# Performance work log

Measured on AMD Instinct MI355X. Metric: run time of the kernel, lower is better.

## Reference

```python
import math
import jax, jax.numpy as jnp
import numpy as np

NUM_HEAD = 16
BLOCK_SIZE = 2048

def get_slopes(n):
    def pow2(n):
        start = 2 ** (-2 ** (-(math.log2(n) - 3)))
        return [start * start ** i for i in range(n)]
    if math.log2(n).is_integer():
        return pow2(n)
    c = 2 ** math.floor(math.log2(n))
    return pow2(c) + get_slopes(2 * c)[0::2][: n - c]

def setup_inputs() -> dict:
    key = jax.random.key(0)
    ks = jax.random.split(key, 5)
    B, T, C = 4, 2048, 1024
    x = jax.random.normal(ks[0], (B, T, C), dtype=jnp.float32)
    Wq = 0.02 * jax.random.normal(ks[1], (C, C), dtype=jnp.float32)
    Wk = 0.02 * jax.random.normal(ks[2], (C, C), dtype=jnp.float32)
    Wv = 0.02 * jax.random.normal(ks[3], (C, C), dtype=jnp.float32)
    Wo = 0.02 * jax.random.normal(ks[4], (C, C), dtype=jnp.float32)
    return {"x": x, "Wq": Wq, "Wk": Wk, "Wv": Wv, "Wo": Wo}

def reference(x, Wq, Wk, Wv, Wo):
    B, T, C = x.shape
    nh, hd = NUM_HEAD, C // NUM_HEAD
    # projections, split heads -> [B, nh, T, hd]
    q = (x @ Wq).reshape(B, T, nh, hd).transpose(0, 2, 1, 3)
    k = (x @ Wk).reshape(B, T, nh, hd).transpose(0, 2, 1, 3)
    v = (x @ Wv).reshape(B, T, nh, hd).transpose(0, 2, 1, 3)
    # full [B, nh, T, T] scores (module materializes these)
    attn = jnp.einsum("bhqd,bhkd->bhqk", q, k) / jnp.sqrt(jnp.float32(hd))
    # ALiBi bias as in create_mask: slope * (j - (block_size - 1)), key-position only
    slopes = jnp.asarray(get_slopes(nh), dtype=jnp.float32)  # [nh]
    bias = slopes[:, None] * (jnp.arange(T, dtype=jnp.float32) - (BLOCK_SIZE - 1))  # [nh, T]
    attn = attn + bias[None, :, None, :]
    # causal mask + stable softmax in fp32
    causal = jnp.tril(jnp.ones((T, T), dtype=bool))
    masked = jnp.where(causal[None, None], attn.astype(jnp.float32), jnp.finfo(jnp.float32).min)
    probs = jax.nn.softmax(masked, axis=-1)
    out = jnp.einsum("bhqk,bhkd->bhqd", probs, v)  # [B, nh, T, hd]
    out = out.transpose(0, 2, 1, 3).reshape(B, T, C)
    return out @ Wo
```

## Files before the change

kernel.cpp:

```cpp
#include <hip/hip_runtime.h>
#include <hip/hip_bf16.h>

#define TSEQ   2048
#define CDIM   1024
#define NHEAD  16
#define HDIM   64

typedef float f32x4  __attribute__((ext_vector_type(4)));
typedef float f32x16v __attribute__((ext_vector_type(16)));
typedef __bf16 bf16x8 __attribute__((ext_vector_type(8)));
typedef unsigned short u16x8 __attribute__((ext_vector_type(8)));
typedef unsigned short u16x4 __attribute__((ext_vector_type(4)));
typedef unsigned int   u32x4 __attribute__((ext_vector_type(4)));

#define QSCALE 0.18033688011112042f
#define LOG2E  1.4426950408889634f

static __device__ __forceinline__ unsigned short f2bf(float f) {
    unsigned u = __builtin_bit_cast(unsigned, f);
    unsigned r = u + 0x7FFFu + ((u >> 16) & 1u);
    return (unsigned short)(r >> 16);
}

static __device__ __forceinline__ f32x4 mfma16(u16x8 a, u16x8 b, f32x4 c) {
    return __builtin_amdgcn_mfma_f32_16x16x32_bf16(
        __builtin_bit_cast(bf16x8, a), __builtin_bit_cast(bf16x8, b), c, 0, 0, 0);
}
static __device__ __forceinline__ f32x16v mfma32(u16x8 a, u16x8 b, f32x16v c) {
    return __builtin_amdgcn_mfma_f32_32x32x16_bf16(
        __builtin_bit_cast(bf16x8, a), __builtin_bit_cast(bf16x8, b), c, 0, 0, 0);
}

static __device__ __forceinline__ void gload16(const void* g, void* l) {
    __builtin_amdgcn_global_load_lds(
        (const __attribute__((address_space(1))) unsigned int*)g,
        (__attribute__((address_space(3))) unsigned int*)l, 16, 0, 0);
}


__global__ __launch_bounds__(256) void castx(
    const float* __restrict__ x, unsigned short* __restrict__ xb)
{
    int t = blockIdx.x * 256 + threadIdx.x;
    f32x4 v = *(const f32x4*)&x[t * 4];
    u16x4 o;
    o[0] = f2bf(v[0]); o[1] = f2bf(v[1]); o[2] = f2bf(v[2]); o[3] = f2bf(v[3]);
    *(u16x4*)&xb[t * 4] = o;
}

__global__ __launch_bounds__(256) void wtcast(
    const float* __restrict__ wq, const float* __restrict__ wk,
    const float* __restrict__ wv, const float* __restrict__ wo,
    unsigned short* __restrict__ wt)
{
    __shared__ unsigned short t[64 * 72];
    const int z = blockIdx.z;
    const float* src = (z == 0) ? wq : (z == 1) ? wk : (z == 2) ? wv : wo;
    const int k0 = blockIdx.x * 64, n0 = blockIdx.y * 64, tid = threadIdx.x;

    #pragma unroll
    for (int i = 0; i < 4; ++i) {
        int idx = i * 256 + tid;
        int r = idx >> 4, c4 = idx & 15;
        f32x4 v = *(const f32x4*)&src[(k0 + r) * 1024 + n0 + c4 * 4];
        u16x4 o;
        o[0] = f2bf(v[0]); o[1] = f2bf(v[1]); o[2] = f2bf(v[2]); o[3] = f2bf(v[3]);
        *(u16x4*)&t[r * 72 + c4 * 4] = o;
    }
    __syncthreads();
    #pragma unroll
    for (int i = 0; i < 2; ++i) {
        int idx = i * 256 + tid;
        int n = idx >> 3, k8 = idx & 7;
        u16x8 o;
        #pragma unroll
        for (int e = 0; e < 8; ++e) o[e] = t[(k8 * 8 + e) * 72 + n];
        *(u16x8*)&wt[z * 1048576 + (n0 + n) * 1024 + k0 + k8 * 8] = o;
    }
}

template<int MODE>
__global__ __launch_bounds__(256) void gemm_gl(
    const unsigned short* __restrict__ A, const unsigned short* __restrict__ WT,
    unsigned short* __restrict__ outb, float* __restrict__ outf)
{
    __shared__ __align__(16) unsigned short Al[128 * 64];
    __shared__ __align__(16) unsigned short Bl[128 * 64];

    const int tid  = threadIdx.x;
    const int z    = blockIdx.z;
    const int m0   = blockIdx.y * 128;
    const int n0   = blockIdx.x * 128;
    const unsigned short* W = WT + (MODE == 0 ? z * 1048576 : 0);

    const int wid  = tid >> 6, lane = tid & 63;
    const int wr   = (wid >> 1) * 64, wc = (wid & 1) * 64;
    const int lrow = lane & 15, lk = (lane >> 4) * 8;

    f32x4 acc[4][4] = {};

    for (int kt = 0; kt < 16; ++kt) {
        __syncthreads();
        #pragma unroll
        for (int c = 0; c < 4; ++c) {
            int cz = wid * 4 + c;
            int row = cz * 8 + (lane >> 3), col = (lane & 7) * 8;
            gload16(&A[(m0 + row) * 1024 + kt * 64 + col], &Al[cz * 512]);
            gload16(&W[(n0 + row) * 1024 + kt * 64 + col], &Bl[cz * 512]);
        }
        __syncthreads();
        #pragma unroll
        for (int ks = 0; ks < 2; ++ks) {
            u16x8 af[4], bfr[4];
            #pragma unroll
            for (int m = 0; m < 4; ++m)
                af[m] = *(const u16x8*)&Al[(wr + m * 16 + lrow) * 64 + ks * 32 + lk];
            #pragma unroll
            for (int n = 0; n < 4; ++n)
                bfr[n] = *(const u16x8*)&Bl[(wc + n * 16 + lrow) * 64 + ks * 32 + lk];
            #pragma unroll
            for (int m = 0; m < 4; ++m)
                #pragma unroll
                for (int n = 0; n < 4; ++n)
                    acc[m][n] = mfma16(af[m], bfr[n], acc[m][n]);
        }
    }

    const int g = lane >> 4;
    #pragma unroll
    for (int m = 0; m < 4; ++m)
        #pragma unroll
        for (int n = 0; n < 4; ++n)
            #pragma unroll
            for (int j = 0; j < 4; ++j) {
                int grow = m0 + wr + m * 16 + g * 4 + j;
                int gcol = n0 + wc + n * 16 + lrow;
                float val = acc[m][n][j];
                if (MODE == 0) {
                    int b = grow >> 11, t = grow & 2047;
                    int h = gcol >> 6,  d = gcol & 63;
                    if (z == 0) val *= QSCALE;
                    if (z == 2)
                        outb[z * 8388608 + (((b << 4) + h) * 64 + d) * 2048 + t] = f2bf(val);
                    else
                        outb[z * 8388608 + (((b << 4) + h) * 2048 + t) * 64 + d] = f2bf(val);
                } else {
                    outf[grow * 1024 + gcol] = val;
                }
            }
}

__global__ __launch_bounds__(512, 2) void attn8w(
    const unsigned short* __restrict__ qh, const unsigned short* __restrict__ kh,
    const unsigned short* __restrict__ vt, unsigned short* __restrict__ aout)
{
    __shared__ __align__(16) unsigned short Kl[2][128 * 64];
    __shared__ __align__(16) unsigned short Vl[2][64 * 128];

    const int j   = blockIdx.x;
    const int bh  = blockIdx.y;
    const int h   = bh & 15, b = bh >> 4;
    const int tid = threadIdx.x, wid = tid >> 6, lane = tid & 63;
    const int l31 = lane & 31, hi = lane >> 5;

    const int cA = 7 - j, cB = j;
    const int ntA = 2 * cA + 2;
    const int nt  = 18;

    const unsigned short* Qb = qh + bh * (TSEQ * HDIM);
    const unsigned short* Kb = kh + bh * (TSEQ * HDIM);
    const unsigned short* Vb = vt + bh * (TSEQ * HDIM);

    const float slope2 = exp2f(-0.5f * (float)(h + 1)) * LOG2E;
    const int   Wwin   = (int)ceilf(40.0f / slope2);

    const int krow = lane >> 3;
    const int kgc  = (lane & 7) ^ krow;
    const int vrow = lane >> 4;
    const int vcc  = lane & 15;

#define STAGE(BUF, KV) do {                                                   \
    _Pragma("unroll")                                                         \
    for (int i_ = 0; i_ < 2; ++i_) {                                          \
        int cz_ = wid * 2 + i_;                                    \
        gload16(&Kb[((KV) + cz_ * 8 + krow) * 64 + kgc * 8],                  \
                &Kl[BUF][cz_ * 512]);                                         \
        int d_ = cz_ * 4 + vrow;                                              \
        int gc_ = vcc ^ (d_ & 15);                                            \
        gload16(&Vb[d_ * 2048 + (KV) + gc_ * 8], &Vl[BUF][cz_ * 512]);        \
    } } while (0)

    int qw = cA * 256 + wid * 32;
    int qg = qw + l31;
    u16x8 qf[4];
    #pragma unroll
    for (int kf = 0; kf < 4; ++kf)
        qf[kf] = *(const u16x8*)&Qb[qg * 64 + kf * 16 + hi * 8];
    float m_r = -1e30f, l_r = 0.f;
    f32x16v Ot[2] = {};

    STAGE(0, 0);
    int cur = 0;

    for (int t = 0; t < nt; ++t) {
        const int kv0 = (t < ntA ? t : t - ntA) * 128;
        __syncthreads();

        if (t + 1 < nt) {
            const int t1 = t + 1;
            STAGE(cur ^ 1, (t1 < ntA ? t1 : t1 - ntA) * 128);
        }

        if (kv0 <= qw + 31 && kv0 + 127 >= qw - Wwin) {
            const int v0 = qw - kv0;
            int nkv2 = (v0 >> 5) + 1; if (nkv2 > 4) nkv2 = 4;
            const bool diag = (kv0 + 127 > qw);

            f32x16v st[4];
            __builtin_amdgcn_s_setprio(1);
            #pragma unroll
            for (int kv2 = 0; kv2 < 4; ++kv2) {
                if (kv2 < nkv2) {
                    f32x16v a = {};
                    #pragma unroll
                    for (int kf = 0; kf < 4; ++kf) {
                        u16x8 ka = *(const u16x8*)&Kl[cur][(kv2 * 32 + l31) * 64 +
                                                           (((kf * 2 + hi) ^ (l31 & 7)) * 8)];
                        a = mfma32(ka, qf[kf], a);
                    }
                    st[kv2] = a;
                } else {
                    st[kv2] = (f32x16v)(-1e30f);
                }
            }
            __builtin_amdgcn_s_setprio(0);

            if (diag) {
                #pragma unroll
                for (int kv2 = 0; kv2 < 4; ++kv2) {
                    if (kv2 < nkv2) {
                        #pragma unroll
                        for (int r = 0; r < 16; ++r) {
                            int kv = kv0 + kv2 * 32 + (r & 3) + 8 * (r >> 2) + 4 * hi;
                            if (kv > qg) st[kv2][r] = -1e30f;
                        }
                    }
                }
            }

            float t16[16];
            #pragma unroll
            for (int i = 0; i < 16; ++i)
                t16[i] = fmaxf(fmaxf(st[0][i], st[1][i]), fmaxf(st[2][i], st[3][i]));
            #pragma unroll
            for (int i = 0; i < 8; ++i) t16[i] = fmaxf(t16[i], t16[i + 8]);
            #pragma unroll
            for (int i = 0; i < 4; ++i) t16[i] = fmaxf(t16[i], t16[i + 4]);
            float rm = fmaxf(fmaxf(t16[0], t16[1]), fmaxf(t16[2], t16[3]));
            rm = fmaxf(rm, __shfl_xor(rm, 32, 64));

            int kvmax = kv0 + 127; if (kvmax > qw + 31) kvmax = qw + 31;
            float cand = rm + slope2 * (float)(kvmax - 2047);

            if (!__all(cand - m_r <= 8.0f)) {
                float mn = fmaxf(m_r, cand);
                float alpha = exp2f(m_r - mn);
                m_r = mn;
                l_r *= alpha;
                Ot[0] *= alpha;
                Ot[1] *= alpha;
            }

            unsigned pku[4][8];
            float s16[16] = {};
            #pragma unroll
            for (int kv2 = 0; kv2 < 4; ++kv2) {
                if (kv2 < nkv2) {
                    float base2 = slope2 * (float)(kv0 + kv2 * 32 + 4 * hi - 2047) - m_r;
                    #pragma unroll
                    for (int r = 0; r < 16; ++r) {
                        float koff = (float)((r & 3) + 8 * (r >> 2));
                        st[kv2][r] = exp2f(st[kv2][r] + fmaf(slope2, koff, base2));
                        s16[r] += st[kv2][r];
                    }
                    #pragma unroll
                    for (int idx = 0; idx < 8; ++idx) {
                        unsigned lo2 = __builtin_bit_cast(unsigned short, (__bf16)st[kv2][2 * idx]);
                        unsigned hh = __builtin_bit_cast(unsigned short, (__bf16)st[kv2][2 * idx + 1]);
                        pku[kv2][idx] = lo2 | (hh << 16);
                    }
                }
            }
            #pragma unroll
            for (int i = 0; i < 8; ++i) s16[i] += s16[i + 8];
            #pragma unroll
            for (int i = 0; i < 4; ++i) s16[i] += s16[i + 4];
            float rs = (s16[0] + s16[1]) + (s16[2] + s16[3]);
            rs += __shfl_xor(rs, 32, 64);
            l_r += rs;

            __builtin_amdgcn_s_setprio(1);
            #pragma unroll
            for (int kf = 0; kf < 8; ++kf) {
                if ((kf >> 1) < nkv2) {
                    const int kv2 = kf >> 1, base = 4 * (kf & 1);
                    unsigned s0 = hi ? pku[kv2][base + 0] : pku[kv2][base + 2];
                    unsigned s1 = hi ? pku[kv2][base + 1] : pku[kv2][base + 3];
                    unsigned r0 = __shfl_xor(s0, 32, 64);
                    unsigned r1 = __shfl_xor(s1, 32, 64);
                    u32x4 w;
                    w[0] = hi ? r0 : pku[kv2][base + 0];
                    w[1] = hi ? r1 : pku[kv2][base + 1];
                    w[2] = hi ? pku[kv2][base + 2] : r0;
                    w[3] = hi ? pku[kv2][base + 3] : r1;
                    u16x8 pb = __builtin_bit_cast(u16x8, w);
                    #pragma unroll
                    for (int dn = 0; dn < 2; ++dn) {
                        u16x8 va = *(const u16x8*)&Vl[cur][(dn * 32 + l31) * 128 +
                                                           (((kf * 2 + hi) ^ (l31 & 15)) * 8)];
                        Ot[dn] = mfma32(va, pb, Ot[dn]);
                    }
                }
            }
            __builtin_amdgcn_s_setprio(0);
        }

        if (t == ntA - 1) {
            float rl = 1.0f / l_r;
            #pragma unroll
            for (int dn = 0; dn < 2; ++dn)
                #pragma unroll
                for (int rq = 0; rq < 4; ++rq) {
                    u16x4 o;
                    #pragma unroll
                    for (int jj = 0; jj < 4; ++jj)
                        o[jj] = f2bf(Ot[dn][rq * 4 + jj] * rl);
                    int d = dn * 32 + 8 * rq + 4 * hi;
                    *(u16x4*)&aout[(b * 2048 + qg) * 1024 + h * 64 + d] = o;
                }
            qw = cB * 256 + wid * 32;
            qg = qw + l31;
            #pragma unroll
            for (int kf = 0; kf < 4; ++kf)
                qf[kf] = *(const u16x8*)&Qb[qg * 64 + kf * 16 + hi * 8];
            m_r = -1e30f; l_r = 0.f;
            Ot[0] = (f32x16v){};
            Ot[1] = (f32x16v){};
        }

        cur ^= 1;
    }

    float rl = 1.0f / l_r;
    #pragma unroll
    for (int dn = 0; dn < 2; ++dn)
        #pragma unroll
        for (int rq = 0; rq < 4; ++rq) {
            u16x4 o;
            #pragma unroll
            for (int jj = 0; jj < 4; ++jj)
                o[jj] = f2bf(Ot[dn][rq * 4 + jj] * rl);
            int d = dn * 32 + 8 * rq + 4 * hi;
            *(u16x4*)&aout[(b * 2048 + qg) * 1024 + h * 64 + d] = o;
        }
#undef STAGE
}

extern "C" void kernel_launch(void* const* d_in, const int* in_sizes, int n_in,
                              void* d_out, int out_size, void* d_ws, size_t ws_size,
                              hipStream_t stream)
{
    const float* x  = (const float*)d_in[0];
    const float* Wq = (const float*)d_in[1];
    const float* Wk = (const float*)d_in[2];
    const float* Wv = (const float*)d_in[3];
    const float* Wo = (const float*)d_in[4];

    unsigned short* ws = (unsigned short*)d_ws;
    unsigned short* wb = ws;
    unsigned short* xb = ws + 4194304;
    unsigned short* qh = ws + 12582912;
    unsigned short* kh = qh + 8388608;
    unsigned short* vt = kh + 8388608;
    unsigned short* ao = xb;

    castx<<<dim3(8192), dim3(256), 0, stream>>>(x, xb);
    wtcast<<<dim3(16, 16, 4), dim3(256), 0, stream>>>(Wq, Wk, Wv, Wo, wb);
    gemm_gl<0><<<dim3(8, 64, 3), dim3(256), 0, stream>>>(xb, wb, qh, (float*)nullptr);
    attn8w<<<dim3(4, 64), dim3(512), 0, stream>>>(qh, kh, vt, ao);
    gemm_gl<1><<<dim3(8, 64, 1), dim3(256), 0, stream>>>(
        ao, wb + 3 * 1048576, (unsigned short*)nullptr, (float*)d_out);
}
```

Measured before the change: 228.9 us.

## Split attention into one chunk per block and skip out-of-window KV tiles

Replaces the paired-chunk attention kernel (each block processes two query chunks across a fixed 18 KV tiles) with one chunk per block over an 8x64 grid. The KV loop starts at the first tile inside the ALiBi window, so tiles that were previously staged but unused are no longer loaded. This removes wasted loads and iterations at the cost of less balanced per-block work and more blocks.

```diff
diff --git a/kernel.cpp b/kernel.cpp
--- a/kernel.cpp
+++ b/kernel.cpp
@@ -150,22 +150,18 @@
             }
 }
 
-__global__ __launch_bounds__(512, 2) void attn8w(
+__global__ __launch_bounds__(512, 2) void attn8s(
     const unsigned short* __restrict__ qh, const unsigned short* __restrict__ kh,
     const unsigned short* __restrict__ vt, unsigned short* __restrict__ aout)
 {
     __shared__ __align__(16) unsigned short Kl[2][128 * 64];
     __shared__ __align__(16) unsigned short Vl[2][64 * 128];
 
-    const int j   = blockIdx.x;
     const int bh  = blockIdx.y;
     const int h   = bh & 15, b = bh >> 4;
+    const int c   = (bh < 32) ? (7 - (int)blockIdx.x) : (int)blockIdx.x;
     const int tid = threadIdx.x, wid = tid >> 6, lane = tid & 63;
     const int l31 = lane & 31, hi = lane >> 5;
-
-    const int cA = 7 - j, cB = j;
-    const int ntA = 2 * cA + 2;
-    const int nt  = 18;
 
     const unsigned short* Qb = qh + bh * (TSEQ * HDIM);
     const unsigned short* Kb = kh + bh * (TSEQ * HDIM);
@@ -173,6 +169,13 @@
 
     const float slope2 = exp2f(-0.5f * (float)(h + 1)) * LOG2E;
     const int   Wwin   = (int)ceilf(40.0f / slope2);
+
+    int blo = c * 256 - Wwin;
+    const int t0     = (blo > 0) ? (blo >> 7) : 0;
+    const int t_last = 2 * c + 1;
+
+    const int qw = c * 256 + wid * 32;
+    const int qg = qw + l31;
 
     const int krow = lane >> 3;
     const int kgc  = (lane & 7) ^ krow;
@@ -190,8 +193,6 @@
         gload16(&Vb[d_ * 2048 + (KV) + gc_ * 8], &Vl[BUF][cz_ * 512]);        \
     } } while (0)
 
-    int qw = cA * 256 + wid * 32;
-    int qg = qw + l31;
     u16x8 qf[4];
     #pragma unroll
     for (int kf = 0; kf < 4; ++kf)
@@ -199,17 +200,14 @@
     float m_r = -1e30f, l_r = 0.f;
     f32x16v Ot[2] = {};
 
-    STAGE(0, 0);
+    STAGE(0, t0 * 128);
     int cur = 0;
 
-    for (int t = 0; t < nt; ++t) {
-        const int kv0 = (t < ntA ? t : t - ntA) * 128;
+    for (int t = t0; t <= t_last; ++t) {
+        const int kv0 = t * 128;
         __syncthreads();
 
-        if (t + 1 < nt) {
-            const int t1 = t + 1;
-            STAGE(cur ^ 1, (t1 < ntA ? t1 : t1 - ntA) * 128);
-        }
+        if (t < t_last) STAGE(cur ^ 1, (t + 1) * 128);
 
         if (kv0 <= qw + 31 && kv0 + 127 >= qw - Wwin) {
             const int v0 = qw - kv0;
@@ -325,29 +323,6 @@
             __builtin_amdgcn_s_setprio(0);
         }
 
-        if (t == ntA - 1) {
-            float rl = 1.0f / l_r;
-            #pragma unroll
-            for (int dn = 0; dn < 2; ++dn)
-                #pragma unroll
-                for (int rq = 0; rq < 4; ++rq) {
-                    u16x4 o;
-                    #pragma unroll
-                    for (int jj = 0; jj < 4; ++jj)
-                        o[jj] = f2bf(Ot[dn][rq * 4 + jj] * rl);
-                    int d = dn * 32 + 8 * rq + 4 * hi;
-                    *(u16x4*)&aout[(b * 2048 + qg) * 1024 + h * 64 + d] = o;
-                }
-            qw = cB * 256 + wid * 32;
-            qg = qw + l31;
-            #pragma unroll
-            for (int kf = 0; kf < 4; ++kf)
-                qf[kf] = *(const u16x8*)&Qb[qg * 64 + kf * 16 + hi * 8];
-            m_r = -1e30f; l_r = 0.f;
-            Ot[0] = (f32x16v){};
-            Ot[1] = (f32x16v){};
-        }
-
         cur ^= 1;
     }
 
@@ -387,7 +362,7 @@
     castx<<<dim3(8192), dim3(256), 0, stream>>>(x, xb);
     wtcast<<<dim3(16, 16, 4), dim3(256), 0, stream>>>(Wq, Wk, Wv, Wo, wb);
     gemm_gl<0><<<dim3(8, 64, 3), dim3(256), 0, stream>>>(xb, wb, qh, (float*)nullptr);
-    attn8w<<<dim3(4, 64), dim3(512), 0, stream>>>(qh, kh, vt, ao);
+    attn8s<<<dim3(8, 64), dim3(512), 0, stream>>>(qh, kh, vt, ao);
     gemm_gl<1><<<dim3(8, 64, 1), dim3(256), 0, stream>>>(
         ao, wb + 3 * 1048576, (unsigned short*)nullptr, (float*)d_out);
 }
```

Result: no change. 227.4 us (-0.7%).
